# Performance work log

Measured on AMD Instinct MI355X. Metric: run time of the kernel, lower is better.

## Reference

```python
import jax, jax.numpy as jnp
import numpy as np

B, C, H, W = 64, 2048, 14, 14
D, S, ITERS, EPS, HID = 256, 8, 3, 1e-8, 512


def build_pos(h, w, d):
    gy, gx = np.meshgrid(np.arange(h), np.arange(w), indexing='ij')
    q = d // 4
    omega = 1.0 / (10000.0 ** (np.arange(q) / q))
    ey = gy.reshape(-1, 1) * omega
    ex = gx.reshape(-1, 1) * omega
    pe = np.concatenate([np.sin(ey), np.cos(ey), np.sin(ex), np.cos(ex)], axis=1)
    return jnp.asarray(pe[None], jnp.float32)  # (1, h*w, d)


def layernorm(x, g, b, eps=1e-5):
    m = x.mean(-1, keepdims=True)
    v = ((x - m) ** 2).mean(-1, keepdims=True)
    return (x - m) * jax.lax.rsqrt(v + eps) * g + b


def setup_inputs() -> dict:
    key = jax.random.key(0)
    ks = jax.random.split(key, 16)
    w = lambda k, shp, s=0.02: jax.random.normal(k, shp, jnp.float32) * s
    inp = {
        'x': jax.random.normal(ks[0], (B, C, H, W), jnp.float32),
        'slot_noise': jax.random.normal(ks[1], (B, S, D), jnp.float32),
        'conv_w': w(ks[2], (C, D)), 'conv_b': jnp.zeros((D,), jnp.float32),
        'pos': build_pos(H, W, D),
        'slots_mu': jax.random.normal(ks[3], (1, 1, D), jnp.float32),
        'slots_logsigma': -jnp.ones((1, 1, D), jnp.float32),
        'qw': w(ks[4], (D, D)), 'qb': jnp.zeros((D,), jnp.float32),
        'kw': w(ks[5], (D, D)), 'kb': jnp.zeros((D,), jnp.float32),
        'vw': w(ks[6], (D, D)), 'vb': jnp.zeros((D,), jnp.float32),
        'gru_wih': w(ks[7], (D, 3 * D)), 'gru_whh': w(ks[8], (D, 3 * D)),
        'gru_bih': jnp.zeros((3 * D,), jnp.float32), 'gru_bhh': jnp.zeros((3 * D,), jnp.float32),
        'w1': w(ks[9], (D, HID)), 'b1': jnp.zeros((HID,), jnp.float32),
        'w2': w(ks[10], (HID, D)), 'b2': jnp.zeros((D,), jnp.float32),
        'ln_in_g': jnp.ones((D,), jnp.float32), 'ln_in_b': jnp.zeros((D,), jnp.float32),
        'ln_s_g': jnp.ones((D,), jnp.float32), 'ln_s_b': jnp.zeros((D,), jnp.float32),
        'ln_ff_g': jnp.ones((D,), jnp.float32), 'ln_ff_b': jnp.zeros((D,), jnp.float32),
    }
    return inp


def reference(x, slot_noise, conv_w, conv_b, pos, slots_mu, slots_logsigma,
              qw, qb, kw, kb, vw, vb, gru_wih, gru_whh, gru_bih, gru_bhh,
              w1, b1, w2, b2, ln_in_g, ln_in_b, ln_s_g, ln_s_b, ln_ff_g, ln_ff_b):
    b, c, h, w_ = x.shape
    d = qw.shape[0]
    scale = d ** (-0.5)
    # (B,C,H,W) -> (B,N,C) -> project -> add pos
    xt = x.transpose(0, 2, 3, 1).reshape(b, h * w_, c)
    xt = xt @ conv_w + conv_b + pos
    # slot init
    slots = slots_mu + jnp.exp(slots_logsigma) * slot_noise  # (B,S,D)
    inp = layernorm(xt, ln_in_g, ln_in_b)
    k = inp @ kw + kb
    v = inp @ vw + vb
    attn = None
    for _ in range(ITERS):
        slots_prev = slots
        s = layernorm(slots, ln_s_g, ln_s_b)
        q = s @ qw + qb
        dots = jnp.einsum('bid,bjd->bij', q, k) * scale  # (B,S,N)
        attn = jax.nn.softmax(dots, axis=1) + EPS  # softmax over slots
        attn = attn / attn.sum(-1, keepdims=True)  # renormalize over keys
        updates = jnp.einsum('bjd,bij->bid', v, attn)  # (B,S,D)
        # GRUCell (torch semantics)
        gi = updates @ gru_wih + gru_bih
        gh = slots_prev @ gru_whh + gru_bhh
        ir, iz, inn = jnp.split(gi, 3, axis=-1)
        hr, hz, hn = jnp.split(gh, 3, axis=-1)
        r = jax.nn.sigmoid(ir + hr)
        z = jax.nn.sigmoid(iz + hz)
        nn_ = jnp.tanh(inn + r * hn)
        slots = (1.0 - z) * nn_ + z * slots_prev
        ff = layernorm(slots, ln_ff_g, ln_ff_b)
        slots = slots + (jax.nn.relu(ff @ w1 + b1)) @ w2 + b2
    attn_map = attn.reshape(b, S, h, w_)
    return slots, attn_map
```

## Files before the change

### kernel.cpp

```cpp
#include <hip/hip_runtime.h>
#include <stdint.h>

#define HWN 196
#define CIN 2048
#define DD  256
#define BB  64
#define NSLOT 8
#define KVPAD 224
#define MTOT 12544

typedef __attribute__((ext_vector_type(8))) short short8;
typedef __attribute__((ext_vector_type(4))) float f32x4;
typedef __attribute__((ext_vector_type(4))) unsigned short us4;

__device__ __forceinline__ ushort f2bf(float f){ union{float f;uint32_t u;}v;v.f=f;uint32_t u=v.u;return (ushort)((u+0x7FFFu+((u>>16)&1u))>>16);}
__device__ __forceinline__ float bf2f(ushort h){ union{uint32_t u;float f;}v;v.u=((uint32_t)h)<<16;return v.f;}
__device__ __forceinline__ float sigm(float x){ return 1.f/(1.f+expf(-x)); }

__device__ __forceinline__ short8 ldsY(const ushort* buf, int LD, int kt, int lane){
    int row = lane & 15;
    int ch = kt*4 + (lane>>4);
    return *(const short8*)&buf[row*LD + ((ch ^ (row&7))<<3)];
}
__device__ __forceinline__ short8 gX(const ushort* base, int K, int nrow, int kt, int lane){
    return *(const short8*)&base[(size_t)nrow*K + kt*32 + (lane>>4)*8];
}

struct TD { const float* s; ushort* d; int R, C, t0; };
struct TD8 { TD a[8]; };

__global__ __launch_bounds__(256) void k_prep(TD8 td){
    __shared__ float tile[32][33];
    int bt = blockIdx.x;
    int mi = 0;
    #pragma unroll
    for (int i = 1; i < 8; ++i) if (bt >= td.a[i].t0) mi = i;
    TD d = td.a[mi];
    int lt = bt - d.t0;
    int tilesx = (d.C + 31) >> 5;
    int cb = (lt % tilesx) * 32, rb = (lt / tilesx) * 32;
    int tx = threadIdx.x & 31, ty = threadIdx.x >> 5;
    for (int i = ty; i < 32; i += 8) {
        int r = rb + i, c = cb + tx;
        tile[i][tx] = (r < d.R && c < d.C) ? d.s[(size_t)r * d.C + c] : 0.f;
    }
    __syncthreads();
    for (int i = ty; i < 32; i += 8) {
        int c = cb + i, r = rb + tx;
        if (c < d.C && r < d.R) d.d[(size_t)c * d.R + r] = f2bf(tile[tx][i]);
    }
}

__global__ __launch_bounds__(512) void k_proj(const float* __restrict__ x,
        const ushort* __restrict__ bT, const float* __restrict__ cb,
        const float* __restrict__ pos, ushort* __restrict__ xt){
    __shared__ ushort As[2][64*64];
    __shared__ ushort Bs[2][128*64];
    const int t = threadIdx.x, lane = t & 63, wv = t >> 6;
    const int wm = wv >> 2, wn = wv & 3;
    const int bm = blockIdx.y * 64;
    const int bn = blockIdx.x * 128;

    const int am = t & 63, akg = t >> 6;
    const int mg = bm + am;
    const int ab = mg / HWN, ap = mg % HWN;
    const float* aptr = x + (size_t)ab * (CIN * HWN) + ap;

    const int bnl = t >> 2;
    const int bch0 = (t & 3) * 2;
    const ushort* bptr = bT + (size_t)(bn + bnl) * CIN;

    f32x4 acc[2][2] = {};
    float areg[8];
    short8 breg[2];

    #pragma unroll
    for (int j = 0; j < 8; ++j) areg[j] = aptr[(size_t)(akg*8+j)*HWN];
    #pragma unroll
    for (int c = 0; c < 2; ++c) breg[c] = *(const short8*)&bptr[(bch0+c)*8];
    {
        short8 av;
        #pragma unroll
        for (int j = 0; j < 8; ++j) av[j] = (short)f2bf(areg[j]);
        *(short8*)&As[0][am*64 + ((akg^(am&7))<<3)] = av;
        #pragma unroll
        for (int c = 0; c < 2; ++c){
            int ch = bch0 + c;
            *(short8*)&Bs[0][bnl*64 + ((ch^(bnl&7))<<3)] = breg[c];
        }
    }
    __syncthreads();
    int cur = 0;
    for (int kt = 0; kt < 32; ++kt){
        int k0n = (kt+1)*64;
        if (kt < 31){
            #pragma unroll
            for (int j = 0; j < 8; ++j) areg[j] = aptr[(size_t)(k0n + akg*8+j)*HWN];
            #pragma unroll
            for (int c = 0; c < 2; ++c) breg[c] = *(const short8*)&bptr[k0n + (bch0+c)*8];
        }
        #pragma unroll
        for (int kk = 0; kk < 2; ++kk){
            short8 afr[2], bfr[2];
            #pragma unroll
            for (int mi = 0; mi < 2; ++mi){
                int row = wm*32 + mi*16 + (lane&15);
                int ch = kk*4 + (lane>>4);
                afr[mi] = *(const short8*)&As[cur][row*64 + ((ch^(row&7))<<3)];
            }
            #pragma unroll
            for (int ni = 0; ni < 2; ++ni){
                int row = wn*32 + ni*16 + (lane&15);
                int ch = kk*4 + (lane>>4);
                bfr[ni] = *(const short8*)&Bs[cur][row*64 + ((ch^(row&7))<<3)];
            }
            #pragma unroll
            for (int mi = 0; mi < 2; ++mi)
                #pragma unroll
                for (int ni = 0; ni < 2; ++ni)
                    acc[mi][ni] = __builtin_amdgcn_mfma_f32_16x16x32_bf16(afr[mi], bfr[ni], acc[mi][ni], 0,0,0);
        }
        if (kt < 31){
            short8 av;
            #pragma unroll
            for (int j = 0; j < 8; ++j) av[j] = (short)f2bf(areg[j]);
            *(short8*)&As[cur^1][am*64 + ((akg^(am&7))<<3)] = av;
            #pragma unroll
            for (int c = 0; c < 2; ++c){
                int ch = bch0 + c;
                *(short8*)&Bs[cur^1][bnl*64 + ((ch^(bnl&7))<<3)] = breg[c];
            }
        }
        __syncthreads();
        cur ^= 1;
    }
    #pragma unroll
    for (int mi = 0; mi < 2; ++mi){
        #pragma unroll
        for (int ni = 0; ni < 2; ++ni){
            int n = bn + wn*32 + ni*16 + (lane&15);
            float cbn = cb[n];
            #pragma unroll
            for (int r = 0; r < 4; ++r){
                int row = wm*32 + mi*16 + (lane>>4)*4 + r;
                int m = bm + row;
                int p = m % HWN;
                xt[(size_t)m*DD + n] = f2bf(acc[mi][ni][r] + cbn + pos[(size_t)p*DD + n]);
            }
        }
    }
}

__global__ __launch_bounds__(512) void k_kv(const ushort* __restrict__ xt,
        const ushort* __restrict__ kwT, const ushort* __restrict__ vwT,
        const float* __restrict__ kb, const float* __restrict__ vb,
        const float* __restrict__ lng, const float* __restrict__ lnb,
        ushort* __restrict__ kbf, ushort* __restrict__ vT){
    __shared__ ushort As[32*256];
    const int t = threadIdx.x, lane = t & 63, wv = t >> 6;
    const int b = blockIdx.x / 7, pblk = blockIdx.x % 7;
    {
        int row = t >> 4, seg = t & 15;
        int grow = b*HWN + pblk*32 + row;
        if (grow > MTOT-1) grow = MTOT-1;
        const ushort* src = &xt[(size_t)grow*DD + seg*16];
        short8 v0 = *(const short8*)&src[0];
        short8 v1 = *(const short8*)&src[8];
        float f[16];
        #pragma unroll
        for (int j = 0; j < 8; ++j){ f[j] = bf2f((ushort)v0[j]); f[8+j] = bf2f((ushort)v1[j]); }
        float s = 0.f, sq = 0.f;
        #pragma unroll
        for (int j = 0; j < 16; ++j){ s += f[j]; sq += f[j]*f[j]; }
        #pragma unroll
        for (int m = 8; m >= 1; m >>= 1){ s += __shfl_xor(s, m, 64); sq += __shfl_xor(sq, m, 64); }
        float mean = s * (1.f/256.f);
        float rs = rsqrtf(sq*(1.f/256.f) - mean*mean + 1e-5f);
        int d0 = seg*16;
        short8 o0, o1;
        #pragma unroll
        for (int j = 0; j < 8; ++j){
            o0[j] = (short)f2bf((f[j]   - mean)*rs*lng[d0+j]   + lnb[d0+j]);
            o1[j] = (short)f2bf((f[8+j] - mean)*rs*lng[d0+8+j] + lnb[d0+8+j]);
        }
        int ch0 = seg*2;
        *(short8*)&As[row*256 + ((ch0^(row&7))<<3)] = o0;
        *(short8*)&As[row*256 + (((ch0+1)^(row&7))<<3)] = o1;
    }
    __syncthreads();
    f32x4 acck[2][2] = {}, accv[2][2] = {};
    const int n0 = wv*32;
    #pragma unroll
    for (int kt = 0; kt < 8; ++kt){
        short8 afr[2];
        #pragma unroll
        for (int mi = 0; mi < 2; ++mi){
            int row = mi*16 + (lane&15);
            int ch = kt*4 + (lane>>4);
            afr[mi] = *(const short8*)&As[row*256 + ((ch^(row&7))<<3)];
        }
        #pragma unroll
        for (int ni = 0; ni < 2; ++ni){
            int n = n0 + ni*16 + (lane&15);
            int koff = kt*32 + (lane>>4)*8;
            short8 bk = *(const short8*)&kwT[(size_t)n*DD + koff];
            short8 bv = *(const short8*)&vwT[(size_t)n*DD + koff];
            #pragma unroll
            for (int mi = 0; mi < 2; ++mi){
                acck[mi][ni] = __builtin_amdgcn_mfma_f32_16x16x32_bf16(afr[mi], bk, acck[mi][ni],0,0,0);
                accv[mi][ni] = __builtin_amdgcn_mfma_f32_16x16x32_bf16(afr[mi], bv, accv[mi][ni],0,0,0);
            }
        }
    }
    #pragma unroll
    for (int mi = 0; mi < 2; ++mi){
        #pragma unroll
        for (int ni = 0; ni < 2; ++ni){
            int n = n0 + ni*16 + (lane&15);
            float kbn = kb[n], vbn = vb[n];
            int pl0 = pblk*32 + mi*16 + (lane>>4)*4;
            us4 pk;
            #pragma unroll
            for (int r = 0; r < 4; ++r){
                kbf[((size_t)b*KVPAD + pl0 + r)*DD + n] = f2bf(acck[mi][ni][r] + kbn);
                pk[r] = f2bf(accv[mi][ni][r] + vbn);
            }
            *(us4*)&vT[((size_t)b*DD + n)*KVPAD + pl0] = pk;
        }
    }
}

__global__ __launch_bounds__(512) void k_init(const float* __restrict__ noise,
        const float* __restrict__ mu, const float* __restrict__ lsig,
        const ushort* __restrict__ qwT, const float* __restrict__ qb,
        const float* __restrict__ gs, const float* __restrict__ bs,
        float* __restrict__ slots, ushort* __restrict__ qbuf){
    __shared__ float Sld[16*256];
    __shared__ ushort Ysn[16*256];
    __shared__ float part[8][16][2];
    __shared__ float stats[16][2];
    const int t = threadIdx.x, lane = t & 63, w = t >> 6;
    const int bb = blockIdx.x, rbase = bb*16;
    {
        int row = t>>5, ch = t&31; int d = ch*8;
        f32x4 n0 = *(const f32x4*)&noise[(size_t)(rbase+row)*DD + d];
        f32x4 n1 = *(const f32x4*)&noise[(size_t)(rbase+row)*DD + d + 4];
        f32x4 m0 = *(const f32x4*)&mu[d];
        f32x4 m1 = *(const f32x4*)&mu[d+4];
        f32x4 l0 = *(const f32x4*)&lsig[d];
        f32x4 l1 = *(const f32x4*)&lsig[d+4];
        f32x4 s0, s1;
        #pragma unroll
        for (int j = 0; j < 4; ++j){
            s0[j] = m0[j] + expf(l0[j])*n0[j];
            s1[j] = m1[j] + expf(l1[j])*n1[j];
        }
        *(f32x4*)&slots[(size_t)(rbase+row)*DD + d] = s0;
        *(f32x4*)&slots[(size_t)(rbase+row)*DD + d + 4] = s1;
        *(f32x4*)&Sld[row*256 + d] = s0;
        *(f32x4*)&Sld[row*256 + d + 4] = s1;
    }
    __syncthreads();
    f32x4 sv[2];
    #pragma unroll
    for (int sub = 0; sub < 2; ++sub){
        int d0 = w*32 + sub*16 + (lane>>4)*4;
        sv[sub] = *(const f32x4*)&Sld[(lane&15)*256 + d0];
    }
    {
        float lsum = 0.f, lsq = 0.f;
        #pragma unroll
        for (int sub = 0; sub < 2; ++sub)
            #pragma unroll
            for (int r = 0; r < 4; ++r){ float v = sv[sub][r]; lsum += v; lsq += v*v; }
        lsum += __shfl_xor(lsum, 16, 64); lsum += __shfl_xor(lsum, 32, 64);
        lsq  += __shfl_xor(lsq, 16, 64);  lsq  += __shfl_xor(lsq, 32, 64);
        if (lane < 16){ part[w][lane][0] = lsum; part[w][lane][1] = lsq; }
    }
    __syncthreads();
    if (t < 16){
        float a = 0.f, c = 0.f;
        #pragma unroll
        for (int i = 0; i < 8; ++i){ a += part[i][t][0]; c += part[i][t][1]; }
        float mean = a*(1.f/256.f);
        stats[t][0] = mean;
        stats[t][1] = rsqrtf(c*(1.f/256.f) - mean*mean + 1e-5f);
    }
    __syncthreads();
    {
        int slot = lane&15;
        float mean = stats[slot][0], rs = stats[slot][1];
        #pragma unroll
        for (int sub = 0; sub < 2; ++sub){
            int d0 = w*32 + sub*16 + (lane>>4)*4;
            f32x4 g4 = *(const f32x4*)&gs[d0];
            f32x4 b4 = *(const f32x4*)&bs[d0];
            us4 o;
            #pragma unroll
            for (int r = 0; r < 4; ++r) o[r] = f2bf((sv[sub][r]-mean)*rs*g4[r] + b4[r]);
            int ch = d0>>3;
            *(us4*)&Ysn[slot*256 + ((ch^(slot&7))<<3) + (d0&7)] = o;
        }
    }
    __syncthreads();
    f32x4 qa[2] = {};
    #pragma unroll
    for (int kt = 0; kt < 8; ++kt){
        short8 ysn = ldsY(Ysn, 256, kt, lane);
        #pragma unroll
        for (int sub = 0; sub < 2; ++sub){
            int nrow = w*32 + sub*16 + (lane&15);
            short8 xx = gX(qwT, 256, nrow, kt, lane);
            qa[sub] = __builtin_amdgcn_mfma_f32_16x16x32_bf16(xx, ysn, qa[sub], 0,0,0);
        }
    }
    #pragma unroll
    for (int sub = 0; sub < 2; ++sub){
        int qd0 = w*32 + sub*16 + (lane>>4)*4;
        f32x4 qb4 = *(const f32x4*)&qb[qd0];
        us4 o;
        #pragma unroll
        for (int r = 0; r < 4; ++r) o[r] = f2bf((qa[sub][r]+qb4[r])*0.0625f);
        *(us4*)&qbuf[(size_t)(rbase+(lane&15))*DD + qd0] = o;
    }
}

__global__ __launch_bounds__(512) void k_slot(
        const ushort* __restrict__ qbuf, const ushort* __restrict__ kbf,
        const ushort* __restrict__ vT, float* __restrict__ slots,
        ushort* __restrict__ qout,
        const ushort* __restrict__ wihT, const ushort* __restrict__ whhT,
        const float* __restrict__ bih, const float* __restrict__ bhh,
        const ushort* __restrict__ w1T, const float* __restrict__ b1,
        const ushort* __restrict__ w2T, const float* __restrict__ b2,
        const float* __restrict__ gff, const float* __restrict__ bff,
        const float* __restrict__ gs, const float* __restrict__ bs,
        const ushort* __restrict__ qwT, const float* __restrict__ qb,
        float* __restrict__ out_slots, float* __restrict__ out_attn,
        int final_){
    __shared__ ushort Yq[16*256];
    __shared__ ushort Xat[16*256];
    __shared__ ushort Yupd[16*256];
    __shared__ ushort Yslb[16*256];
    __shared__ ushort Ysn[16*256];
    __shared__ ushort Yh[16*512];
    __shared__ float wpart[8][16];
    __shared__ float invk[16];
    __shared__ float part[8][16][2];
    __shared__ float stats[16][2];
    const int t = threadIdx.x, lane = t & 63, w = t >> 6;
    const int b = blockIdx.x;
    const int rbase = b * NSLOT;
    const int srow = lane & 15;
    const int srd = (srow < NSLOT) ? srow : 0;

    if (t < 256){
        int row = t>>5, ch = t&31;
        short8 v = *(const short8*)&qbuf[(size_t)(rbase+row)*DD + ch*8];
        *(short8*)&Yq[row*256 + ((ch^(row&7))<<3)] = v;
        f32x4 s0 = *(const f32x4*)&slots[(size_t)(rbase+row)*DD + ch*8];
        f32x4 s1 = *(const f32x4*)&slots[(size_t)(rbase+row)*DD + ch*8 + 4];
        short8 sv;
        #pragma unroll
        for (int j = 0; j < 4; ++j){ sv[j] = (short)f2bf(s0[j]); sv[4+j] = (short)f2bf(s1[j]); }
        *(short8*)&Yslb[row*256 + ((ch^(row&7))<<3)] = sv;
    } else {
        int i = t - 256;
        int row = (i>>5) + 8, ch = i&31;
        short8 z;
        #pragma unroll
        for (int j = 0; j < 8; ++j) z[j] = 0;
        *(short8*)&Yq[row*256 + ((ch^(row&7))<<3)] = z;
        *(short8*)&Yupd[row*256 + ((ch^(row&7))<<3)] = z;
        *(short8*)&Yslb[row*256 + ((ch^(row&7))<<3)] = z;
    }
    __syncthreads();
    {
        short8 yf[8];
        #pragma unroll
        for (int kt = 0; kt < 8; ++kt) yf[kt] = ldsY(Yq, 256, kt, lane);
        float ps = 0.f;
        #pragma unroll
        for (int rep = 0; rep < 2; ++rep){
            int f = w + rep*8;
            if (f < 14){
                f32x4 acc = {};
                #pragma unroll
                for (int kt = 0; kt < 8; ++kt){
                    short8 xx = gX(kbf + (size_t)b*KVPAD*DD, 256, f*16 + (lane&15), kt, lane);
                    acc = __builtin_amdgcn_mfma_f32_16x16x32_bf16(xx, yf[kt], acc, 0,0,0);
                }
                int k0 = f*16 + (lane>>4)*4;
                us4 o;
                #pragma unroll
                for (int r = 0; r < 4; ++r){
                    float v = acc[r];
                    float mx = v;
                    mx = fmaxf(mx, __shfl_xor(mx, 1, 64));
                    mx = fmaxf(mx, __shfl_xor(mx, 2, 64));
                    mx = fmaxf(mx, __shfl_xor(mx, 4, 64));
                    float e = expf(v - mx);
                    float se = e;
                    se += __shfl_xor(se, 1, 64);
                    se += __shfl_xor(se, 2, 64);
                    se += __shfl_xor(se, 4, 64);
                    float val = e/se + 1e-8f;
                    if (k0 + r >= HWN) val = 0.f;
                    ps += val;
                    o[r] = f2bf(val);
                }
                int ch = k0 >> 3;
                *(us4*)&Xat[srow*256 + ((ch^(srow&7))<<3) + (k0&7)] = o;
            }
        }
        ps += __shfl_xor(ps, 16, 64);
        ps += __shfl_xor(ps, 32, 64);
        if (lane < 16) wpart[w][lane] = ps;
    }
    __syncthreads();
    if (t < 16){
        float s = 0.f;
        #pragma unroll
        for (int i = 0; i < 8; ++i) s += wpart[i][t];
        invk[t] = 1.f/s;
    }
    __syncthreads();
    {
        short8 xa[7];
        #pragma unroll
        for (int kt = 0; kt < 7; ++kt) xa[kt] = ldsY(Xat, 256, kt, lane);
        f32x4 iv = *(const f32x4*)&invk[(lane>>4)*4];
        #pragma unroll
        for (int i = 0; i < 2; ++i){
            int d0 = (w*2 + i)*16;
            f32x4 acc = {};
            #pragma unroll
            for (int kt = 0; kt < 7; ++kt){
                short8 y = gX(vT + (size_t)b*DD*KVPAD, KVPAD, d0 + (lane&15), kt, lane);
                acc = __builtin_amdgcn_mfma_f32_16x16x32_bf16(xa[kt], y, acc, 0,0,0);
            }
            #pragma unroll
            for (int r = 0; r < 4; ++r){
                int s2 = (lane>>4)*4 + r;
                if (s2 < NSLOT){
                    int d = d0 + (lane&15);
                    int ch = d >> 3;
                    Yupd[s2*256 + ((ch^(s2&7))<<3) + (d&7)] = f2bf(acc[r]*iv[r]);
                }
            }
        }
    }
    if (final_){
        for (int idx = t; idx < NSLOT*HWN; idx += 512){
            int slot = idx/HWN, key = idx - slot*HWN;
            int ch = key >> 3;
            out_attn[(size_t)b*NSLOT*HWN + idx] =
                bf2f(Xat[slot*256 + ((ch^(slot&7))<<3) + (key&7)]) * invk[slot];
        }
    }
    __syncthreads();
    f32x4 gi[6] = {}, gh[6] = {};
    #pragma unroll
    for (int kt = 0; kt < 8; ++kt){
        short8 yu = ldsY(Yupd, 256, kt, lane);
        short8 ys = ldsY(Yslb, 256, kt, lane);
        #pragma unroll
        for (int g = 0; g < 3; ++g)
            #pragma unroll
            for (int sub = 0; sub < 2; ++sub){
                int nrow = g*256 + w*32 + sub*16 + (lane&15);
                short8 xi = gX(wihT, 256, nrow, kt, lane);
                short8 xh = gX(whhT, 256, nrow, kt, lane);
                gi[g*2+sub] = __builtin_amdgcn_mfma_f32_16x16x32_bf16(xi, yu, gi[g*2+sub], 0,0,0);
                gh[g*2+sub] = __builtin_amdgcn_mfma_f32_16x16x32_bf16(xh, ys, gh[g*2+sub], 0,0,0);
            }
    }
    f32x4 snew[2];
    #pragma unroll
    for (int sub = 0; sub < 2; ++sub){
        int d0 = w*32 + sub*16 + (lane>>4)*4;
        f32x4 sp  = *(const f32x4*)&slots[(size_t)(rbase + srd)*DD + d0];
        f32x4 bir = *(const f32x4*)&bih[d0];
        f32x4 biz = *(const f32x4*)&bih[256 + d0];
        f32x4 bin = *(const f32x4*)&bih[512 + d0];
        f32x4 bhr = *(const f32x4*)&bhh[d0];
        f32x4 bhz = *(const f32x4*)&bhh[256 + d0];
        f32x4 bhn = *(const f32x4*)&bhh[512 + d0];
        #pragma unroll
        for (int r = 0; r < 4; ++r){
            float ir = gi[0+sub][r] + bir[r];
            float iz = gi[2+sub][r] + biz[r];
            float in_ = gi[4+sub][r] + bin[r];
            float hr = gh[0+sub][r] + bhr[r];
            float hz = gh[2+sub][r] + bhz[r];
            float hn = gh[4+sub][r] + bhn[r];
            float rr = sigm(ir + hr);
            float zz = sigm(iz + hz);
            float nn = tanhf(in_ + rr*hn);
            snew[sub][r] = (1.f - zz)*nn + zz*sp[r];
        }
    }
    {
        float lsum = 0.f, lsq = 0.f;
        #pragma unroll
        for (int sub = 0; sub < 2; ++sub)
            #pragma unroll
            for (int r = 0; r < 4; ++r){ float v = snew[sub][r]; lsum += v; lsq += v*v; }
        lsum += __shfl_xor(lsum, 16, 64); lsum += __shfl_xor(lsum, 32, 64);
        lsq  += __shfl_xor(lsq, 16, 64);  lsq  += __shfl_xor(lsq, 32, 64);
        if (lane < 16){ part[w][lane][0] = lsum; part[w][lane][1] = lsq; }
    }
    __syncthreads();
    if (t < 16){
        float a = 0.f, c = 0.f;
        #pragma unroll
        for (int i = 0; i < 8; ++i){ a += part[i][t][0]; c += part[i][t][1]; }
        float mean = a*(1.f/256.f);
        stats[t][0] = mean;
        stats[t][1] = rsqrtf(c*(1.f/256.f) - mean*mean + 1e-5f);
    }
    __syncthreads();
    {
        float mean = stats[srow][0], rs = stats[srow][1];
        #pragma unroll
        for (int sub = 0; sub < 2; ++sub){
            int d0 = w*32 + sub*16 + (lane>>4)*4;
            f32x4 g4 = *(const f32x4*)&gff[d0];
            f32x4 b4 = *(const f32x4*)&bff[d0];
            us4 o;
            #pragma unroll
            for (int r = 0; r < 4; ++r) o[r] = f2bf((snew[sub][r]-mean)*rs*g4[r] + b4[r]);
            int ch = d0 >> 3;
            *(us4*)&Ysn[srow*256 + ((ch^(srow&7))<<3) + (d0&7)] = o;
        }
    }
    __syncthreads();
    {
        f32x4 hh[4] = {};
        #pragma unroll
        for (int kt = 0; kt < 8; ++kt){
            short8 ysn = ldsY(Ysn, 256, kt, lane);
            #pragma unroll
            for (int s2 = 0; s2 < 4; ++s2){
                int nrow = w*64 + s2*16 + (lane&15);
                short8 xx = gX(w1T, 256, nrow, kt, lane);
                hh[s2] = __builtin_amdgcn_mfma_f32_16x16x32_bf16(xx, ysn, hh[s2], 0,0,0);
            }
        }
        #pragma unroll
        for (int s2 = 0; s2 < 4; ++s2){
            int n0 = w*64 + s2*16 + (lane>>4)*4;
            f32x4 b14 = *(const f32x4*)&b1[n0];
            us4 o;
            #pragma unroll
            for (int r = 0; r < 4; ++r) o[r] = f2bf(fmaxf(hh[s2][r] + b14[r], 0.f));
            int ch = n0 >> 3;
            *(us4*)&Yh[srow*512 + ((ch^(srow&7))<<3) + (n0&7)] = o;
        }
    }
    __syncthreads();
    f32x4 ns[2];
    {
        f32x4 o2[2] = {};
        #pragma unroll
        for (int kt = 0; kt < 16; ++kt){
            short8 yh = ldsY(Yh, 512, kt, lane);
            #pragma unroll
            for (int sub = 0; sub < 2; ++sub){
                int nrow = w*32 + sub*16 + (lane&15);
                short8 xx = gX(w2T, 512, nrow, kt, lane);
                o2[sub] = __builtin_amdgcn_mfma_f32_16x16x32_bf16(xx, yh, o2[sub], 0,0,0);
            }
        }
        float* dst = final_ ? out_slots : slots;
        #pragma unroll
        for (int sub = 0; sub < 2; ++sub){
            int d0 = w*32 + sub*16 + (lane>>4)*4;
            f32x4 b24 = *(const f32x4*)&b2[d0];
            #pragma unroll
            for (int r = 0; r < 4; ++r) ns[sub][r] = o2[sub][r] + b24[r] + snew[sub][r];
            if (srow < NSLOT)
                *(f32x4*)&dst[(size_t)(rbase + srow)*DD + d0] = ns[sub];
        }
    }
    if (final_) return;
    {
        float lsum = 0.f, lsq = 0.f;
        #pragma unroll
        for (int sub = 0; sub < 2; ++sub)
            #pragma unroll
            for (int r = 0; r < 4; ++r){ float v = ns[sub][r]; lsum += v; lsq += v*v; }
        lsum += __shfl_xor(lsum, 16, 64); lsum += __shfl_xor(lsum, 32, 64);
        lsq  += __shfl_xor(lsq, 16, 64);  lsq  += __shfl_xor(lsq, 32, 64);
        if (lane < 16){ part[w][lane][0] = lsum; part[w][lane][1] = lsq; }
    }
    __syncthreads();
    if (t < 16){
        float a = 0.f, c = 0.f;
        #pragma unroll
        for (int i = 0; i < 8; ++i){ a += part[i][t][0]; c += part[i][t][1]; }
        float mean = a*(1.f/256.f);
        stats[t][0] = mean;
        stats[t][1] = rsqrtf(c*(1.f/256.f) - mean*mean + 1e-5f);
    }
    __syncthreads();
    {
        float mean = stats[srow][0], rs = stats[srow][1];
        #pragma unroll
        for (int sub = 0; sub < 2; ++sub){
            int d0 = w*32 + sub*16 + (lane>>4)*4;
            f32x4 g4 = *(const f32x4*)&gs[d0];
            f32x4 b4 = *(const f32x4*)&bs[d0];
            us4 o;
            #pragma unroll
            for (int r = 0; r < 4; ++r) o[r] = f2bf((ns[sub][r]-mean)*rs*g4[r] + b4[r]);
            int ch = d0 >> 3;
            *(us4*)&Ysn[srow*256 + ((ch^(srow&7))<<3) + (d0&7)] = o;
        }
    }
    __syncthreads();
    {
        f32x4 qa[2] = {};
        #pragma unroll
        for (int kt = 0; kt < 8; ++kt){
            short8 ysn = ldsY(Ysn, 256, kt, lane);
            #pragma unroll
            for (int sub = 0; sub < 2; ++sub){
                int nrow = w*32 + sub*16 + (lane&15);
                short8 xx = gX(qwT, 256, nrow, kt, lane);
                qa[sub] = __builtin_amdgcn_mfma_f32_16x16x32_bf16(xx, ysn, qa[sub], 0,0,0);
            }
        }
        #pragma unroll
        for (int sub = 0; sub < 2; ++sub){
            int qd0 = w*32 + sub*16 + (lane>>4)*4;
            f32x4 qb4 = *(const f32x4*)&qb[qd0];
            us4 o;
            #pragma unroll
            for (int r = 0; r < 4; ++r) o[r] = f2bf((qa[sub][r]+qb4[r])*0.0625f);
            if (srow < NSLOT)
                *(us4*)&qout[(size_t)(rbase + srow)*DD + qd0] = o;
        }
    }
}

extern "C" void kernel_launch(void* const* d_in, const int* in_sizes, int n_in,
                              void* d_out, int out_size, void* d_ws, size_t ws_size,
                              hipStream_t stream) {
    const float* x      = (const float*)d_in[0];
    const float* noise  = (const float*)d_in[1];
    const float* conv_w = (const float*)d_in[2];
    const float* conv_b = (const float*)d_in[3];
    const float* pos    = (const float*)d_in[4];
    const float* mu     = (const float*)d_in[5];
    const float* logsig = (const float*)d_in[6];
    const float* qw  = (const float*)d_in[7];
    const float* qb  = (const float*)d_in[8];
    const float* kw  = (const float*)d_in[9];
    const float* kb  = (const float*)d_in[10];
    const float* vw  = (const float*)d_in[11];
    const float* vb  = (const float*)d_in[12];
    const float* wih = (const float*)d_in[13];
    const float* whh = (const float*)d_in[14];
    const float* bih = (const float*)d_in[15];
    const float* bhh = (const float*)d_in[16];
    const float* w1  = (const float*)d_in[17];
    const float* b1  = (const float*)d_in[18];
    const float* w2  = (const float*)d_in[19];
    const float* b2  = (const float*)d_in[20];
    const float* g_in = (const float*)d_in[21];
    const float* b_in = (const float*)d_in[22];
    const float* g_s  = (const float*)d_in[23];
    const float* b_s  = (const float*)d_in[24];
    const float* g_ff = (const float*)d_in[25];
    const float* b_ff = (const float*)d_in[26];

    char* w = (char*)d_ws;
    ushort* xt     = (ushort*)w; w += (size_t)MTOT*DD*2;
    ushort* kbf    = (ushort*)w; w += (size_t)BB*KVPAD*DD*2;
    ushort* vT     = (ushort*)w; w += (size_t)BB*DD*KVPAD*2;
    ushort* cwT    = (ushort*)w; w += (size_t)DD*CIN*2;
    ushort* qwT    = (ushort*)w; w += (size_t)DD*DD*2;
    ushort* kwT    = (ushort*)w; w += (size_t)DD*DD*2;
    ushort* vwT    = (ushort*)w; w += (size_t)DD*DD*2;
    ushort* wihT   = (ushort*)w; w += (size_t)768*DD*2;
    ushort* whhT   = (ushort*)w; w += (size_t)768*DD*2;
    ushort* w1T    = (ushort*)w; w += (size_t)512*DD*2;
    ushort* w2T    = (ushort*)w; w += (size_t)DD*512*2;
    ushort* qbb    = (ushort*)w; w += (size_t)BB*NSLOT*DD*2;
    float*  slotsb = (float*)w;  w += (size_t)BB*NSLOT*DD*4;

    float* out_slots = (float*)d_out;
    float* out_attn  = (float*)d_out + (size_t)BB*NSLOT*DD;

    TD8 td;
    td.a[0] = { conv_w, cwT, 2048, 256,    0 };
    td.a[1] = { qw,     qwT,  256, 256,  512 };
    td.a[2] = { kw,     kwT,  256, 256,  576 };
    td.a[3] = { vw,     vwT,  256, 256,  640 };
    td.a[4] = { wih,    wihT, 256, 768,  704 };
    td.a[5] = { whh,    whhT, 256, 768,  896 };
    td.a[6] = { w1,     w1T,  256, 512, 1088 };
    td.a[7] = { w2,     w2T,  512, 256, 1216 };

    k_prep<<<1344, 256, 0, stream>>>(td);
    k_proj<<<dim3(2, 196), 512, 0, stream>>>(x, cwT, conv_b, pos, xt);
    k_kv<<<448, 512, 0, stream>>>(xt, kwT, vwT, kb, vb, g_in, b_in, kbf, vT);
    k_init<<<32, 512, 0, stream>>>(noise, mu, logsig, qwT, qb, g_s, b_s, slotsb, qbb);
    for (int it = 0; it < 3; ++it){
        k_slot<<<BB, 512, 0, stream>>>(qbb, kbf, vT, slotsb, qbb,
                                       wihT, whhT, bih, bhh, w1T, b1, w2T, b2,
                                       g_ff, b_ff, g_s, b_s, qwT, qb,
                                       out_slots, out_attn, it == 2);
    }
}
```

Before: 243.1 us.

## Fuse input projection, layernorm and K/V projection into one kernel

Merges the conv projection kernel and the K/V kernel into a single kernel where each block computes all 256 output channels for 32 rows. LayerNorm is applied in-register via a cross-wave reduction, and the K/V GEMMs run from LDS. This removes the bf16 intermediate round-trip through global memory and reads the large input tensor once instead of twice. Conv weights are read directly from global/L2 instead of staged in LDS, which may add L2 traffic, and padding rows of the K/V buffers are no longer written.

```diff
diff --git a/kernel.cpp b/kernel.cpp
--- a/kernel.cpp
+++ b/kernel.cpp
@@ -51,68 +51,58 @@
     }
 }
 
-__global__ __launch_bounds__(512) void k_proj(const float* __restrict__ x,
-        const ushort* __restrict__ bT, const float* __restrict__ cb,
-        const float* __restrict__ pos, ushort* __restrict__ xt){
-    __shared__ ushort As[2][64*64];
-    __shared__ ushort Bs[2][128*64];
+__global__ __launch_bounds__(512, 8) void k_projkv(const float* __restrict__ x,
+        const ushort* __restrict__ cwT, const float* __restrict__ cb,
+        const float* __restrict__ pos, const float* __restrict__ lng,
+        const float* __restrict__ lnb,
+        const ushort* __restrict__ kwT, const ushort* __restrict__ vwT,
+        const float* __restrict__ kb, const float* __restrict__ vb,
+        ushort* __restrict__ kbf, ushort* __restrict__ vT){
+    __shared__ ushort As[2][32*64];
+    __shared__ ushort Asn[32*256];
+    __shared__ float lnpart[32][8][2];
+    __shared__ float stats[32][2];
     const int t = threadIdx.x, lane = t & 63, wv = t >> 6;
-    const int wm = wv >> 2, wn = wv & 3;
-    const int bm = blockIdx.y * 64;
-    const int bn = blockIdx.x * 128;
-
-    const int am = t & 63, akg = t >> 6;
+    const int bm = blockIdx.x * 32;
+
+    const int am = t & 31, kg = t >> 5;
     const int mg = bm + am;
     const int ab = mg / HWN, ap = mg % HWN;
     const float* aptr = x + (size_t)ab * (CIN * HWN) + ap;
 
-    const int bnl = t >> 2;
-    const int bch0 = (t & 3) * 2;
-    const ushort* bptr = bT + (size_t)(bn + bnl) * CIN;
-
     f32x4 acc[2][2] = {};
-    float areg[8];
-    short8 breg[2];
-
-    #pragma unroll
-    for (int j = 0; j < 8; ++j) areg[j] = aptr[(size_t)(akg*8+j)*HWN];
-    #pragma unroll
-    for (int c = 0; c < 2; ++c) breg[c] = *(const short8*)&bptr[(bch0+c)*8];
-    {
-        short8 av;
-        #pragma unroll
-        for (int j = 0; j < 8; ++j) av[j] = (short)f2bf(areg[j]);
-        *(short8*)&As[0][am*64 + ((akg^(am&7))<<3)] = av;
-        #pragma unroll
-        for (int c = 0; c < 2; ++c){
-            int ch = bch0 + c;
-            *(short8*)&Bs[0][bnl*64 + ((ch^(bnl&7))<<3)] = breg[c];
-        }
+    float areg[4];
+
+    #pragma unroll
+    for (int j = 0; j < 4; ++j) areg[j] = aptr[(size_t)(kg*4+j)*HWN];
+    {
+        us4 av;
+        #pragma unroll
+        for (int j = 0; j < 4; ++j) av[j] = f2bf(areg[j]);
+        int ch = kg >> 1;
+        *(us4*)&As[0][am*64 + ((ch^(am&7))<<3) + (kg&1)*4] = av;
     }
     __syncthreads();
     int cur = 0;
     for (int kt = 0; kt < 32; ++kt){
-        int k0n = (kt+1)*64;
         if (kt < 31){
             #pragma unroll
-            for (int j = 0; j < 8; ++j) areg[j] = aptr[(size_t)(k0n + akg*8+j)*HWN];
-            #pragma unroll
-            for (int c = 0; c < 2; ++c) breg[c] = *(const short8*)&bptr[k0n + (bch0+c)*8];
+            for (int j = 0; j < 4; ++j)
+                areg[j] = aptr[(size_t)((kt+1)*64 + kg*4+j)*HWN];
         }
         #pragma unroll
         for (int kk = 0; kk < 2; ++kk){
             short8 afr[2], bfr[2];
             #pragma unroll
             for (int mi = 0; mi < 2; ++mi){
-                int row = wm*32 + mi*16 + (lane&15);
+                int row = mi*16 + (lane&15);
                 int ch = kk*4 + (lane>>4);
                 afr[mi] = *(const short8*)&As[cur][row*64 + ((ch^(row&7))<<3)];
             }
             #pragma unroll
             for (int ni = 0; ni < 2; ++ni){
-                int row = wn*32 + ni*16 + (lane&15);
-                int ch = kk*4 + (lane>>4);
-                bfr[ni] = *(const short8*)&Bs[cur][row*64 + ((ch^(row&7))<<3)];
+                int n = wv*32 + ni*16 + (lane&15);
+                bfr[ni] = *(const short8*)&cwT[(size_t)n*CIN + kt*64 + kk*32 + (lane>>4)*8];
             }
             #pragma unroll
             for (int mi = 0; mi < 2; ++mi)
@@ -121,15 +111,11 @@
                     acc[mi][ni] = __builtin_amdgcn_mfma_f32_16x16x32_bf16(afr[mi], bfr[ni], acc[mi][ni], 0,0,0);
         }
         if (kt < 31){
-            short8 av;
-            #pragma unroll
-            for (int j = 0; j < 8; ++j) av[j] = (short)f2bf(areg[j]);
-            *(short8*)&As[cur^1][am*64 + ((akg^(am&7))<<3)] = av;
-            #pragma unroll
-            for (int c = 0; c < 2; ++c){
-                int ch = bch0 + c;
-                *(short8*)&Bs[cur^1][bnl*64 + ((ch^(bnl&7))<<3)] = breg[c];
-            }
+            us4 av;
+            #pragma unroll
+            for (int j = 0; j < 4; ++j) av[j] = f2bf(areg[j]);
+            int ch = kg >> 1;
+            *(us4*)&As[cur^1][am*64 + ((ch^(am&7))<<3) + (kg&1)*4] = av;
         }
         __syncthreads();
         cur ^= 1;
@@ -137,59 +123,49 @@
     #pragma unroll
     for (int mi = 0; mi < 2; ++mi){
         #pragma unroll
+        for (int r = 0; r < 4; ++r){
+            int row = mi*16 + (lane>>4)*4 + r;
+            int p = (bm + row) % HWN;
+            float s = 0.f, ss = 0.f;
+            #pragma unroll
+            for (int ni = 0; ni < 2; ++ni){
+                int n = wv*32 + ni*16 + (lane&15);
+                float v = acc[mi][ni][r] + cb[n] + pos[(size_t)p*DD + n];
+                acc[mi][ni][r] = v;
+                s += v; ss += v*v;
+            }
+            #pragma unroll
+            for (int m = 8; m >= 1; m >>= 1){ s += __shfl_xor(s, m, 64); ss += __shfl_xor(ss, m, 64); }
+            if ((lane & 15) == 0){ lnpart[row][wv][0] = s; lnpart[row][wv][1] = ss; }
+        }
+    }
+    __syncthreads();
+    if (t < 32){
+        float a = 0.f, c = 0.f;
+        #pragma unroll
+        for (int i = 0; i < 8; ++i){ a += lnpart[t][i][0]; c += lnpart[t][i][1]; }
+        float mean = a * (1.f/256.f);
+        stats[t][0] = mean;
+        stats[t][1] = rsqrtf(c*(1.f/256.f) - mean*mean + 1e-5f);
+    }
+    __syncthreads();
+    #pragma unroll
+    for (int mi = 0; mi < 2; ++mi){
+        #pragma unroll
         for (int ni = 0; ni < 2; ++ni){
-            int n = bn + wn*32 + ni*16 + (lane&15);
-            float cbn = cb[n];
+            int n = wv*32 + ni*16 + (lane&15);
+            float gn = lng[n], bn = lnb[n];
             #pragma unroll
             for (int r = 0; r < 4; ++r){
-                int row = wm*32 + mi*16 + (lane>>4)*4 + r;
-                int m = bm + row;
-                int p = m % HWN;
-                xt[(size_t)m*DD + n] = f2bf(acc[mi][ni][r] + cbn + pos[(size_t)p*DD + n]);
-            }
-        }
-    }
-}
-
-__global__ __launch_bounds__(512) void k_kv(const ushort* __restrict__ xt,
-        const ushort* __restrict__ kwT, const ushort* __restrict__ vwT,
-        const float* __restrict__ kb, const float* __restrict__ vb,
-        const float* __restrict__ lng, const float* __restrict__ lnb,
-        ushort* __restrict__ kbf, ushort* __restrict__ vT){
-    __shared__ ushort As[32*256];
-    const int t = threadIdx.x, lane = t & 63, wv = t >> 6;
-    const int b = blockIdx.x / 7, pblk = blockIdx.x % 7;
-    {
-        int row = t >> 4, seg = t & 15;
-        int grow = b*HWN + pblk*32 + row;
-        if (grow > MTOT-1) grow = MTOT-1;
-        const ushort* src = &xt[(size_t)grow*DD + seg*16];
-        short8 v0 = *(const short8*)&src[0];
-        short8 v1 = *(const short8*)&src[8];
-        float f[16];
-        #pragma unroll
-        for (int j = 0; j < 8; ++j){ f[j] = bf2f((ushort)v0[j]); f[8+j] = bf2f((ushort)v1[j]); }
-        float s = 0.f, sq = 0.f;
-        #pragma unroll
-        for (int j = 0; j < 16; ++j){ s += f[j]; sq += f[j]*f[j]; }
-        #pragma unroll
-        for (int m = 8; m >= 1; m >>= 1){ s += __shfl_xor(s, m, 64); sq += __shfl_xor(sq, m, 64); }
-        float mean = s * (1.f/256.f);
-        float rs = rsqrtf(sq*(1.f/256.f) - mean*mean + 1e-5f);
-        int d0 = seg*16;
-        short8 o0, o1;
-        #pragma unroll
-        for (int j = 0; j < 8; ++j){
-            o0[j] = (short)f2bf((f[j]   - mean)*rs*lng[d0+j]   + lnb[d0+j]);
-            o1[j] = (short)f2bf((f[8+j] - mean)*rs*lng[d0+8+j] + lnb[d0+8+j]);
-        }
-        int ch0 = seg*2;
-        *(short8*)&As[row*256 + ((ch0^(row&7))<<3)] = o0;
-        *(short8*)&As[row*256 + (((ch0+1)^(row&7))<<3)] = o1;
+                int row = mi*16 + (lane>>4)*4 + r;
+                float o = (acc[mi][ni][r] - stats[row][0]) * stats[row][1] * gn + bn;
+                int ch = n >> 3;
+                Asn[row*256 + ((ch^(row&7))<<3) + (n&7)] = f2bf(o);
+            }
+        }
     }
     __syncthreads();
     f32x4 acck[2][2] = {}, accv[2][2] = {};
-    const int n0 = wv*32;
     #pragma unroll
     for (int kt = 0; kt < 8; ++kt){
         short8 afr[2];
@@ -197,11 +173,11 @@
         for (int mi = 0; mi < 2; ++mi){
             int row = mi*16 + (lane&15);
             int ch = kt*4 + (lane>>4);
-            afr[mi] = *(const short8*)&As[row*256 + ((ch^(row&7))<<3)];
+            afr[mi] = *(const short8*)&Asn[row*256 + ((ch^(row&7))<<3)];
         }
         #pragma unroll
         for (int ni = 0; ni < 2; ++ni){
-            int n = n0 + ni*16 + (lane&15);
+            int n = wv*32 + ni*16 + (lane&15);
             int koff = kt*32 + (lane>>4)*8;
             short8 bk = *(const short8*)&kwT[(size_t)n*DD + koff];
             short8 bv = *(const short8*)&vwT[(size_t)n*DD + koff];
@@ -216,16 +192,17 @@
     for (int mi = 0; mi < 2; ++mi){
         #pragma unroll
         for (int ni = 0; ni < 2; ++ni){
-            int n = n0 + ni*16 + (lane&15);
+            int n = wv*32 + ni*16 + (lane&15);
             float kbn = kb[n], vbn = vb[n];
-            int pl0 = pblk*32 + mi*16 + (lane>>4)*4;
+            int m0 = bm + mi*16 + (lane>>4)*4;
+            int bq = m0 / HWN, p0 = m0 % HWN;
             us4 pk;
             #pragma unroll
             for (int r = 0; r < 4; ++r){
-                kbf[((size_t)b*KVPAD + pl0 + r)*DD + n] = f2bf(acck[mi][ni][r] + kbn);
+                kbf[((size_t)bq*KVPAD + p0 + r)*DD + n] = f2bf(acck[mi][ni][r] + kbn);
                 pk[r] = f2bf(accv[mi][ni][r] + vbn);
             }
-            *(us4*)&vT[((size_t)b*DD + n)*KVPAD + pl0] = pk;
+            *(us4*)&vT[((size_t)bq*DD + n)*KVPAD + p0] = pk;
         }
     }
 }
@@ -676,7 +653,6 @@
     const float* b_ff = (const float*)d_in[26];
 
     char* w = (char*)d_ws;
-    ushort* xt     = (ushort*)w; w += (size_t)MTOT*DD*2;
     ushort* kbf    = (ushort*)w; w += (size_t)BB*KVPAD*DD*2;
     ushort* vT     = (ushort*)w; w += (size_t)BB*DD*KVPAD*2;
     ushort* cwT    = (ushort*)w; w += (size_t)DD*CIN*2;
@@ -704,8 +680,8 @@
     td.a[7] = { w2,     w2T,  512, 256, 1216 };
 
     k_prep<<<1344, 256, 0, stream>>>(td);
-    k_proj<<<dim3(2, 196), 512, 0, stream>>>(x, cwT, conv_b, pos, xt);
-    k_kv<<<448, 512, 0, stream>>>(xt, kwT, vwT, kb, vb, g_in, b_in, kbf, vT);
+    k_projkv<<<392, 512, 0, stream>>>(x, cwT, conv_b, pos, g_in, b_in,
+                                      kwT, vwT, kb, vb, kbf, vT);
     k_init<<<32, 512, 0, stream>>>(noise, mu, logsig, qwT, qb, g_s, b_s, slotsb, qbb);
     for (int it = 0; it < 3; ++it){
         k_slot<<<BB, 512, 0, stream>>>(qbb, kbf, vT, slotsb, qbb,
```

New measurement: 258.4 us. 1.06x slower.

## Split-K conv projection with full-N tiles, fuse reduction into LN/KV kernel

Applied to the files above, without the earlier changes.

The 1x1 conv projection now gives each block all 256 output columns for a 64-row tile, so x is read once instead of twice. K is split into two halves across blocks to keep the grid at 392 blocks. Weights are read straight from global/L2 instead of staged through LDS. The two fp32 partial sums go to a new workspace and are added with bias and positional encoding inside the LayerNorm+KV kernel, which adds about 25MB of fp32 partial writes and reads in exchange for halving the x traffic.

```diff
diff --git a/kernel.cpp b/kernel.cpp
--- a/kernel.cpp
+++ b/kernel.cpp
@@ -8,6 +8,7 @@
 #define NSLOT 8
 #define KVPAD 224
 #define MTOT 12544
+#define BKP 128
 
 typedef __attribute__((ext_vector_type(8))) short short8;
 typedef __attribute__((ext_vector_type(4))) float f32x4;
@@ -52,126 +53,120 @@
 }
 
 __global__ __launch_bounds__(512) void k_proj(const float* __restrict__ x,
-        const ushort* __restrict__ bT, const float* __restrict__ cb,
-        const float* __restrict__ pos, ushort* __restrict__ xt){
-    __shared__ ushort As[2][64*64];
-    __shared__ ushort Bs[2][128*64];
+        const ushort* __restrict__ cwT, float* __restrict__ Cpart){
+    __shared__ ushort As[2][64*BKP];
     const int t = threadIdx.x, lane = t & 63, wv = t >> 6;
-    const int wm = wv >> 2, wn = wv & 3;
-    const int bm = blockIdx.y * 64;
-    const int bn = blockIdx.x * 128;
-
-    const int am = t & 63, akg = t >> 6;
+    const int tile = blockIdx.x >> 1, kq = blockIdx.x & 1;
+    const int bm = tile * 64;
+    const int kbase = kq * 1024;
+
+    const int am = t & 63, kg = t >> 6;
     const int mg = bm + am;
     const int ab = mg / HWN, ap = mg % HWN;
-    const float* aptr = x + (size_t)ab * (CIN * HWN) + ap;
-
-    const int bnl = t >> 2;
-    const int bch0 = (t & 3) * 2;
-    const ushort* bptr = bT + (size_t)(bn + bnl) * CIN;
-
-    f32x4 acc[2][2] = {};
-    float areg[8];
-    short8 breg[2];
-
-    #pragma unroll
-    for (int j = 0; j < 8; ++j) areg[j] = aptr[(size_t)(akg*8+j)*HWN];
-    #pragma unroll
-    for (int c = 0; c < 2; ++c) breg[c] = *(const short8*)&bptr[(bch0+c)*8];
-    {
-        short8 av;
-        #pragma unroll
-        for (int j = 0; j < 8; ++j) av[j] = (short)f2bf(areg[j]);
-        *(short8*)&As[0][am*64 + ((akg^(am&7))<<3)] = av;
-        #pragma unroll
-        for (int c = 0; c < 2; ++c){
-            int ch = bch0 + c;
-            *(short8*)&Bs[0][bnl*64 + ((ch^(bnl&7))<<3)] = breg[c];
-        }
+    const float* aptr = x + (size_t)ab*(CIN*HWN) + ap + (size_t)kbase*HWN;
+
+    f32x4 acc[4][2] = {};
+    float areg[16];
+
+    #pragma unroll
+    for (int j = 0; j < 16; ++j) areg[j] = aptr[(size_t)(kg*16+j)*HWN];
+    {
+        short8 av0, av1;
+        #pragma unroll
+        for (int j = 0; j < 8; ++j){ av0[j] = (short)f2bf(areg[j]); av1[j] = (short)f2bf(areg[8+j]); }
+        int ch0 = kg*2;
+        *(short8*)&As[0][am*BKP + ((ch0^(am&7))<<3)] = av0;
+        *(short8*)&As[0][am*BKP + (((ch0+1)^(am&7))<<3)] = av1;
     }
     __syncthreads();
     int cur = 0;
-    for (int kt = 0; kt < 32; ++kt){
-        int k0n = (kt+1)*64;
-        if (kt < 31){
-            #pragma unroll
-            for (int j = 0; j < 8; ++j) areg[j] = aptr[(size_t)(k0n + akg*8+j)*HWN];
-            #pragma unroll
-            for (int c = 0; c < 2; ++c) breg[c] = *(const short8*)&bptr[k0n + (bch0+c)*8];
-        }
-        #pragma unroll
-        for (int kk = 0; kk < 2; ++kk){
-            short8 afr[2], bfr[2];
-            #pragma unroll
-            for (int mi = 0; mi < 2; ++mi){
-                int row = wm*32 + mi*16 + (lane&15);
+    for (int kt = 0; kt < 8; ++kt){
+        if (kt < 7){
+            #pragma unroll
+            for (int j = 0; j < 16; ++j)
+                areg[j] = aptr[(size_t)((kt+1)*BKP + kg*16+j)*HWN];
+        }
+        short8 bfr[4][2];
+        #pragma unroll
+        for (int kk = 0; kk < 4; ++kk)
+            #pragma unroll
+            for (int ni = 0; ni < 2; ++ni){
+                int n = wv*32 + ni*16 + (lane&15);
+                bfr[kk][ni] = *(const short8*)&cwT[(size_t)n*CIN + kbase + kt*BKP + kk*32 + (lane>>4)*8];
+            }
+        #pragma unroll
+        for (int kk = 0; kk < 4; ++kk){
+            short8 afr[4];
+            #pragma unroll
+            for (int mi = 0; mi < 4; ++mi){
+                int row = mi*16 + (lane&15);
                 int ch = kk*4 + (lane>>4);
-                afr[mi] = *(const short8*)&As[cur][row*64 + ((ch^(row&7))<<3)];
-            }
-            #pragma unroll
-            for (int ni = 0; ni < 2; ++ni){
-                int row = wn*32 + ni*16 + (lane&15);
-                int ch = kk*4 + (lane>>4);
-                bfr[ni] = *(const short8*)&Bs[cur][row*64 + ((ch^(row&7))<<3)];
-            }
-            #pragma unroll
-            for (int mi = 0; mi < 2; ++mi)
+                afr[mi] = *(const short8*)&As[cur][row*BKP + ((ch^(row&7))<<3)];
+            }
+            #pragma unroll
+            for (int mi = 0; mi < 4; ++mi)
                 #pragma unroll
                 for (int ni = 0; ni < 2; ++ni)
-                    acc[mi][ni] = __builtin_amdgcn_mfma_f32_16x16x32_bf16(afr[mi], bfr[ni], acc[mi][ni], 0,0,0);
-        }
-        if (kt < 31){
-            short8 av;
-            #pragma unroll
-            for (int j = 0; j < 8; ++j) av[j] = (short)f2bf(areg[j]);
-            *(short8*)&As[cur^1][am*64 + ((akg^(am&7))<<3)] = av;
-            #pragma unroll
-            for (int c = 0; c < 2; ++c){
-                int ch = bch0 + c;
-                *(short8*)&Bs[cur^1][bnl*64 + ((ch^(bnl&7))<<3)] = breg[c];
-            }
+                    acc[mi][ni] = __builtin_amdgcn_mfma_f32_16x16x32_bf16(afr[mi], bfr[kk][ni], acc[mi][ni], 0,0,0);
+        }
+        if (kt < 7){
+            short8 av0, av1;
+            #pragma unroll
+            for (int j = 0; j < 8; ++j){ av0[j] = (short)f2bf(areg[j]); av1[j] = (short)f2bf(areg[8+j]); }
+            int ch0 = kg*2;
+            *(short8*)&As[cur^1][am*BKP + ((ch0^(am&7))<<3)] = av0;
+            *(short8*)&As[cur^1][am*BKP + (((ch0+1)^(am&7))<<3)] = av1;
         }
         __syncthreads();
         cur ^= 1;
     }
-    #pragma unroll
-    for (int mi = 0; mi < 2; ++mi){
+    float* outp = Cpart + (size_t)kq*MTOT*DD;
+    #pragma unroll
+    for (int mi = 0; mi < 4; ++mi){
         #pragma unroll
         for (int ni = 0; ni < 2; ++ni){
-            int n = bn + wn*32 + ni*16 + (lane&15);
-            float cbn = cb[n];
+            int n = wv*32 + ni*16 + (lane&15);
             #pragma unroll
             for (int r = 0; r < 4; ++r){
-                int row = wm*32 + mi*16 + (lane>>4)*4 + r;
-                int m = bm + row;
-                int p = m % HWN;
-                xt[(size_t)m*DD + n] = f2bf(acc[mi][ni][r] + cbn + pos[(size_t)p*DD + n]);
+                int m = bm + mi*16 + (lane>>4)*4 + r;
+                outp[(size_t)m*DD + n] = acc[mi][ni][r];
             }
         }
     }
 }
 
-__global__ __launch_bounds__(512) void k_kv(const ushort* __restrict__ xt,
+__global__ __launch_bounds__(512) void k_red(const float* __restrict__ Cpart,
+        const float* __restrict__ cb, const float* __restrict__ pos,
+        const float* __restrict__ lng, const float* __restrict__ lnb,
         const ushort* __restrict__ kwT, const ushort* __restrict__ vwT,
         const float* __restrict__ kb, const float* __restrict__ vb,
-        const float* __restrict__ lng, const float* __restrict__ lnb,
         ushort* __restrict__ kbf, ushort* __restrict__ vT){
     __shared__ ushort As[32*256];
     const int t = threadIdx.x, lane = t & 63, wv = t >> 6;
     const int b = blockIdx.x / 7, pblk = blockIdx.x % 7;
     {
         int row = t >> 4, seg = t & 15;
-        int grow = b*HWN + pblk*32 + row;
+        int pin = pblk*32 + row;
+        int grow = b*HWN + pin;
         if (grow > MTOT-1) grow = MTOT-1;
-        const ushort* src = &xt[(size_t)grow*DD + seg*16];
-        short8 v0 = *(const short8*)&src[0];
-        short8 v1 = *(const short8*)&src[8];
+        int p = pin < HWN ? pin : HWN-1;
+        const float* c0 = Cpart + (size_t)grow*DD + seg*16;
+        const float* c1 = Cpart + (size_t)MTOT*DD + (size_t)grow*DD + seg*16;
+        const float* pp = pos + (size_t)p*DD + seg*16;
         float f[16];
-        #pragma unroll
-        for (int j = 0; j < 8; ++j){ f[j] = bf2f((ushort)v0[j]); f[8+j] = bf2f((ushort)v1[j]); }
         float s = 0.f, sq = 0.f;
         #pragma unroll
-        for (int j = 0; j < 16; ++j){ s += f[j]; sq += f[j]*f[j]; }
+        for (int q = 0; q < 4; ++q){
+            f32x4 a  = *(const f32x4*)&c0[q*4];
+            f32x4 bq = *(const f32x4*)&c1[q*4];
+            f32x4 pv = *(const f32x4*)&pp[q*4];
+            f32x4 cv = *(const f32x4*)&cb[seg*16 + q*4];
+            #pragma unroll
+            for (int r2 = 0; r2 < 4; ++r2){
+                float v = a[r2] + bq[r2] + pv[r2] + cv[r2];
+                f[q*4+r2] = v; s += v; sq += v*v;
+            }
+        }
         #pragma unroll
         for (int m = 8; m >= 1; m >>= 1){ s += __shfl_xor(s, m, 64); sq += __shfl_xor(sq, m, 64); }
         float mean = s * (1.f/256.f);
@@ -676,7 +671,6 @@
     const float* b_ff = (const float*)d_in[26];
 
     char* w = (char*)d_ws;
-    ushort* xt     = (ushort*)w; w += (size_t)MTOT*DD*2;
     ushort* kbf    = (ushort*)w; w += (size_t)BB*KVPAD*DD*2;
     ushort* vT     = (ushort*)w; w += (size_t)BB*DD*KVPAD*2;
     ushort* cwT    = (ushort*)w; w += (size_t)DD*CIN*2;
@@ -689,6 +683,7 @@
     ushort* w2T    = (ushort*)w; w += (size_t)DD*512*2;
     ushort* qbb    = (ushort*)w; w += (size_t)BB*NSLOT*DD*2;
     float*  slotsb = (float*)w;  w += (size_t)BB*NSLOT*DD*4;
+    float*  Cpart  = (float*)w;  w += (size_t)2*MTOT*DD*4;
 
     float* out_slots = (float*)d_out;
     float* out_attn  = (float*)d_out + (size_t)BB*NSLOT*DD;
@@ -704,8 +699,9 @@
     td.a[7] = { w2,     w2T,  512, 256, 1216 };
 
     k_prep<<<1344, 256, 0, stream>>>(td);
-    k_proj<<<dim3(2, 196), 512, 0, stream>>>(x, cwT, conv_b, pos, xt);
-    k_kv<<<448, 512, 0, stream>>>(xt, kwT, vwT, kb, vb, g_in, b_in, kbf, vT);
+    k_proj<<<392, 512, 0, stream>>>(x, cwT, Cpart);
+    k_red<<<448, 512, 0, stream>>>(Cpart, conv_b, pos, g_in, b_in,
+                                   kwT, vwT, kb, vb, kbf, vT);
     k_init<<<32, 512, 0, stream>>>(noise, mu, logsig, qwT, qb, g_s, b_s, slotsb, qbb);
     for (int it = 0; it < 3; ++it){
         k_slot<<<BB, 512, 0, stream>>>(qbb, kbf, vT, slotsb, qbb,
```

After: 241.2 us. No clear change (-0.8%).
